# Performance work log

Hardware: AMD Instinct MI355X
Metric: run time of the kernel (lower is better)

The kernel has to match this reference:

```python
import jax, jax.numpy as jnp
import numpy as np

B = 16384      # batch
F = 39         # num fields
NUM = 13       # num numerical fields (len(mask_value[0]))
E = 64         # embed_dim
FD = 26000     # per-field vocab size
TOTAL_VOCAB = F * FD


def setup_inputs() -> dict:
    key = jax.random.key(0)
    k = jax.random.split(key, 7)
    features = jax.random.randint(k[0], (B, F), 0, FD)               # per-field ids
    mask = jax.random.randint(k[1], (B, NUM), 0, F)                  # field indices to rescale
    mask_apply = jax.random.randint(k[2], (B, NUM), 0, 2).astype(jnp.bool_)  # True where pd.isnull branch fires
    mask_value = jax.random.uniform(k[3], (B, NUM), dtype=jnp.float32)
    emb_table = jax.random.normal(k[4], (TOTAL_VOCAB, E), dtype=jnp.float32) * 0.01
    lin_w = jax.random.normal(k[5], (E,), dtype=jnp.float32) * 0.01  # FeaturesLinear: Linear(embed_dim, 1)
    lin_b = jnp.zeros((), dtype=jnp.float32)
    return {"features": features, "mask": mask, "mask_apply": mask_apply,
            "mask_value": mask_value, "emb_table": emb_table,
            "lin_w": lin_w, "lin_b": lin_b}


def reference(features, mask, mask_apply, mask_value, emb_table, lin_w, lin_b):
    # FeaturesEmbedding: add per-field offsets, then gather -> (B, F, E)
    offsets = (jnp.arange(F) * FD).astype(features.dtype)
    x = emb_table[features + offsets[None, :]]
    # masked per-row multiply: x[i, mask[i, j]] *= mask_value[i, j] where mask_apply
    scale = jnp.where(mask_apply, mask_value, jnp.float32(1.0))       # (B, NUM)
    bidx = jnp.arange(B)[:, None]                                     # (B, 1)
    x = x.at[bidx, mask].multiply(scale[..., None])                   # scatter-multiply, handles dup indices
    # FeaturesLinear: Linear(E, 1) per field, summed over fields -> (B,)
    logits = jnp.einsum('bfe,e->b', x, lin_w) + jnp.float32(F) * lin_b
    return jax.nn.sigmoid(logits)
```

## Files before the change

kernel.cpp:

```cpp
#include <hip/hip_runtime.h>
#include <hip/hip_bf16.h>

constexpr int Bn   = 16384;
constexpr int Fn   = 39;
constexpr int NUMn = 13;
constexpr int En   = 64;
constexpr int FDn  = 26000;
constexpr int TV   = Fn * FDn;

__global__ __launch_bounds__(256) void dot_precompute(
    const float* __restrict__ emb,
    const float* __restrict__ lin_w,
    float*       __restrict__ d)
{
    const int lane = threadIdx.x & 63;
    const int wid  = (blockIdx.x * blockDim.x + threadIdx.x) >> 6;
    const int s = lane & 15;
    const int g = lane >> 4;

    const float4 w4 = *reinterpret_cast<const float4*>(lin_w + s * 4);
    const int row0 = wid * 16 + g;

    if (row0 + 12 < TV) {
#pragma unroll
        for (int i = 0; i < 4; ++i) {
            const int row = row0 + i * 4;
            const float4 v = *reinterpret_cast<const float4*>(emb + row * En + s * 4);
            float p = v.x * w4.x + v.y * w4.y + v.z * w4.z + v.w * w4.w;
            p += __shfl_xor(p, 1, 64);
            p += __shfl_xor(p, 2, 64);
            p += __shfl_xor(p, 4, 64);
            p += __shfl_xor(p, 8, 64);
            if (s == 0) d[row] = p;
        }
    } else {
#pragma unroll
        for (int i = 0; i < 4; ++i) {
            const int row = row0 + i * 4;
            float p = 0.0f;
            if (row < TV) {
                const float4 v = *reinterpret_cast<const float4*>(emb + row * En + s * 4);
                p = v.x * w4.x + v.y * w4.y + v.z * w4.z + v.w * w4.w;
            }
            p += __shfl_xor(p, 1, 64);
            p += __shfl_xor(p, 2, 64);
            p += __shfl_xor(p, 4, 64);
            p += __shfl_xor(p, 8, 64);
            if (s == 0 && row < TV) d[row] = p;
        }
    }
}

__global__ __launch_bounds__(256) void logits_kernel(
    const int*   __restrict__ features,
    const int*   __restrict__ mask,
    const unsigned char* __restrict__ mask_apply,
    const float* __restrict__ mask_value,
    const float* __restrict__ d,
    const float* __restrict__ lin_b,
    float*       __restrict__ out)
{
    const int lane = threadIdx.x & 63;
    const int row  = blockIdx.x * (blockDim.x >> 6) + (threadIdx.x >> 6);
    if (row >= Bn) return;

    float v = 0.0f;
    if (lane < Fn) {
        const int feat = features[row * Fn + lane];
        const float dv = d[feat + lane * FDn];
        float scale = 1.0f;
#pragma unroll
        for (int n = 0; n < NUMn; ++n) {
            const int   m  = mask[row * NUMn + n];
            const bool  ap = mask_apply[row * NUMn + n] != 0;
            const float mv = mask_value[row * NUMn + n];
            if (m == lane && ap) scale *= mv;
        }
        v = scale * dv;
    }
#pragma unroll
    for (int off = 32; off > 0; off >>= 1)
        v += __shfl_down(v, off, 64);

    if (lane == 0) {
        const float logit = v + (float)Fn * lin_b[0];
        out[row] = 1.0f / (1.0f + expf(-logit));
    }
}

extern "C" void kernel_launch(void* const* d_in, const int* in_sizes, int n_in,
                              void* d_out, int out_size, void* d_ws, size_t ws_size,
                              hipStream_t stream) {
    const int*   features   = (const int*)  d_in[0];
    const int*   mask       = (const int*)  d_in[1];
    const unsigned char* mask_apply = (const unsigned char*)d_in[2];
    const float* mask_value = (const float*)d_in[3];
    const float* emb        = (const float*)d_in[4];
    const float* lin_w      = (const float*)d_in[5];
    const float* lin_b      = (const float*)d_in[6];
    float*       out        = (float*)d_out;
    float*       d          = (float*)d_ws;

    const int blocks1 = (TV + 63) / 64;
    dot_precompute<<<blocks1, 256, 0, stream>>>(emb, lin_w, d);

    const int blocks2 = Bn / 4;
    logits_kernel<<<blocks2, 256, 0, stream>>>(
        features, mask, mask_apply, mask_value, d, lin_b, out);
}
```

Baseline: 371.4 us.

## Compute one embedding row dot product per thread with grid-stride loop

The dot-product precompute now assigns a full 64-element row to each lane, accumulating with FMAs in four partial sums instead of splitting a row over 16 lanes and reducing with shuffles. It launches a fixed 2048-block grid with a grid-stride loop and a launch-bounds occupancy hint. This removes shuffle reductions and per-lane redundant stores. In exchange, adjacent lanes read addresses 256 bytes apart, which weakens memory coalescing on a bandwidth-bound pass.

```diff
diff --git a/kernel.cpp b/kernel.cpp
--- a/kernel.cpp
+++ b/kernel.cpp
@@ -8,45 +8,29 @@
 constexpr int FDn  = 26000;
 constexpr int TV   = Fn * FDn;
 
-__global__ __launch_bounds__(256) void dot_precompute(
+__global__ __launch_bounds__(256, 8) void dot_precompute_v2(
     const float* __restrict__ emb,
     const float* __restrict__ lin_w,
     float*       __restrict__ d)
 {
     const int lane = threadIdx.x & 63;
     const int wid  = (blockIdx.x * blockDim.x + threadIdx.x) >> 6;
-    const int s = lane & 15;
-    const int g = lane >> 4;
+    const int nw   = (gridDim.x * blockDim.x) >> 6;
 
-    const float4 w4 = *reinterpret_cast<const float4*>(lin_w + s * 4);
-    const int row0 = wid * 16 + g;
-
-    if (row0 + 12 < TV) {
+    for (int row0 = wid << 6; row0 < TV; row0 += (nw << 6)) {
+        const int row = row0 + lane;
+        if (row < TV) {
+            const float* p = emb + (size_t)row * En;
+            float4 a = make_float4(0.f, 0.f, 0.f, 0.f);
 #pragma unroll
-        for (int i = 0; i < 4; ++i) {
-            const int row = row0 + i * 4;
-            const float4 v = *reinterpret_cast<const float4*>(emb + row * En + s * 4);
-            float p = v.x * w4.x + v.y * w4.y + v.z * w4.z + v.w * w4.w;
-            p += __shfl_xor(p, 1, 64);
-            p += __shfl_xor(p, 2, 64);
-            p += __shfl_xor(p, 4, 64);
-            p += __shfl_xor(p, 8, 64);
-            if (s == 0) d[row] = p;
-        }
-    } else {
-#pragma unroll
-        for (int i = 0; i < 4; ++i) {
-            const int row = row0 + i * 4;
-            float p = 0.0f;
-            if (row < TV) {
-                const float4 v = *reinterpret_cast<const float4*>(emb + row * En + s * 4);
-                p = v.x * w4.x + v.y * w4.y + v.z * w4.z + v.w * w4.w;
+            for (int j = 0; j < 16; ++j) {
+                const float4 v = *reinterpret_cast<const float4*>(p + j * 4);
+                a.x = fmaf(v.x, lin_w[j * 4 + 0], a.x);
+                a.y = fmaf(v.y, lin_w[j * 4 + 1], a.y);
+                a.z = fmaf(v.z, lin_w[j * 4 + 2], a.z);
+                a.w = fmaf(v.w, lin_w[j * 4 + 3], a.w);
             }
-            p += __shfl_xor(p, 1, 64);
-            p += __shfl_xor(p, 2, 64);
-            p += __shfl_xor(p, 4, 64);
-            p += __shfl_xor(p, 8, 64);
-            if (s == 0 && row < TV) d[row] = p;
+            d[row] = (a.x + a.y) + (a.z + a.w);
         }
     }
 }
@@ -101,10 +85,8 @@
     float*       out        = (float*)d_out;
     float*       d          = (float*)d_ws;
 
-    const int blocks1 = (TV + 63) / 64;
-    dot_precompute<<<blocks1, 256, 0, stream>>>(emb, lin_w, d);
+    dot_precompute_v2<<<2048, 256, 0, stream>>>(emb, lin_w, d);
 
-    const int blocks2 = Bn / 4;
-    logits_kernel<<<blocks2, 256, 0, stream>>>(
+    logits_kernel<<<Bn / 4, 256, 0, stream>>>(
         features, mask, mask_apply, mask_value, d, lin_b, out);
 }
```

Result: slower. 383.1 us (+3.2%).
